# Kernel tuning notes

Measured on AMD Instinct MI355X. Metric: run time of the kernel, lower is better.

## Reference

```python
import jax, jax.numpy as jnp
import numpy as np

B, S, D = 8, 2048, 64
NEG = -1e9


def setup_inputs() -> dict:
    key = jax.random.key(0)
    kq, kk, kv = jax.random.split(key, 3)
    return {
        "queries": jax.random.normal(kq, (B, S, D), dtype=jnp.float32),
        "keys": jax.random.normal(kk, (B, S, D), dtype=jnp.float32),
        "values": jax.random.normal(kv, (B, S, D), dtype=jnp.float32),
        "mask_q": jnp.ones((B, S), dtype=jnp.float32),
        "mask_k": jnp.ones((B, S), dtype=jnp.float32),
        "mask_v": jnp.ones((B, S), dtype=jnp.float32),
    }


def reference(queries, keys, values, mask_q, mask_k, mask_v):
    # scaled QK^T: [B, Sq, Sk]
    scaler = jnp.sqrt(jnp.asarray(queries.shape[-1], dtype=queries.dtype))
    scores = jnp.einsum("bqd,bkd->bqk", queries, keys) / scaler
    # additive padding mask from outer product of query/key masks
    padding_mask = mask_q[:, :, None] * mask_k[:, None, :]  # [B, Sq, Sk]
    scores = scores + (1.0 - padding_mask) * NEG
    attention_weights = jax.nn.softmax(scores, axis=-1)
    # mask values then weighted sum
    values = values * mask_v[:, :, None]
    output = jnp.einsum("bqk,bkd->bqd", attention_weights, values)
    return output
```

## Files before the change

kernel.cpp:

```cpp
#include <hip/hip_runtime.h>
#include <hip/hip_bf16.h>
#include <math.h>

#define BATCH 8
#define SEQ   2048
#define DIM   64
#define NEGC  (-1e9f)
#define SPLIT 4
#define TPB   8

typedef short short8  __attribute__((ext_vector_type(8)));
typedef float f32x4   __attribute__((ext_vector_type(4)));
typedef float f32x16  __attribute__((ext_vector_type(16)));

#define MFMA32(a, b, c) __builtin_amdgcn_mfma_f32_32x32x16_bf16((a), (b), (c), 0, 0, 0)

__device__ __forceinline__ ushort f2bf(float x) {
    uint u = __float_as_uint(x);
    uint r = (u + 0x7fffu + ((u >> 16) & 1u)) >> 16;
    return (ushort)r;
}
__device__ __forceinline__ float bf2f(ushort h) {
    return __uint_as_float(((uint)h) << 16);
}

__global__ __launch_bounds__(256)
void prep_kv(const float* __restrict__ K, const float* __restrict__ V,
             const float* __restrict__ MV, ushort* __restrict__ ws) {
    __shared__ float raw[64 * 68];
    const int t    = threadIdx.x;
    const int b    = blockIdx.x >> 5;
    const int tile = blockIdx.x & 31;
    const float* Kb  = K  + ((size_t)b * SEQ + tile * 64) * DIM;
    const float* Vb  = V  + ((size_t)b * SEQ + tile * 64) * DIM;
    const float* MVb = MV + (size_t)b * SEQ + tile * 64;
    ushort* wsI = ws + (size_t)(b * 32 + tile) * 8192;

#pragma unroll
    for (int u = 0; u < 4; u++) {
        int f = t + 256 * u, key = f >> 4, d4 = (f & 15) * 4;
        *(float4*)&raw[key * 68 + d4] = *(const float4*)(Kb + (size_t)f * 4);
    }
    __syncthreads();
#pragma unroll
    for (int u = 0; u < 2; u++) {
        int r = t + 256 * u;
        int mt = r >> 8, kc = (r >> 6) & 3, L = r & 63;
        int key = mt * 32 + (L & 31), d0 = kc * 16 + (L >> 5) * 8;
        float4 x0 = *(float4*)&raw[key * 68 + d0];
        float4 x1 = *(float4*)&raw[key * 68 + d0 + 4];
        float xs[8] = {x0.x, x0.y, x0.z, x0.w, x1.x, x1.y, x1.z, x1.w};
        short8 hv;
#pragma unroll
        for (int j = 0; j < 8; j++) hv[j] = (short)f2bf(xs[j]);
        *(short8*)(wsI + r * 8) = hv;
    }
    __syncthreads();

#pragma unroll
    for (int u = 0; u < 4; u++) {
        int f = t + 256 * u, key = f >> 4, d4 = (f & 15) * 4;
        float4 x = *(const float4*)(Vb + (size_t)f * 4);
        float mv = MVb[key];
        x.x *= mv; x.y *= mv; x.z *= mv; x.w *= mv;
        *(float4*)&raw[key * 68 + d4] = x;
    }
    __syncthreads();
#pragma unroll
    for (int u = 0; u < 2; u++) {
        int r = t + 256 * u;
        int dt = r >> 8, kc = (r >> 6) & 3, L = r & 63;
        int d = dt * 32 + (L & 31), k0 = kc * 16 + (L >> 5) * 8;
        short8 ov;
#pragma unroll
        for (int j = 0; j < 8; j++) ov[j] = (short)f2bf(raw[(k0 + j) * 68 + d]);
        *(short8*)(wsI + 4096 + r * 8) = ov;
    }
}

__global__ __launch_bounds__(256, 4)
void attn_main(const float* __restrict__ Q, const float* __restrict__ MQ,
               const float* __restrict__ MK, const ushort* __restrict__ ws,
               float* __restrict__ PO, float* __restrict__ ML) {
    __shared__ __align__(16) ushort Stage[2][8192];

    const int t    = threadIdx.x;
    const int w    = t >> 6;
    const int lane = t & 63;
    const int h    = lane >> 5;
    const int lm   = lane & 31;
    const int qg   = w & 1;
    const int kh   = w >> 1;

    const int s  = blockIdx.x & 3;
    const int qb = blockIdx.x >> 2;
    const int b  = qb >> 5;
    const int qt = qb & 31;
    const int q  = qt * 64 + qg * 32 + lm;

    const float*  MKb  = MK + (size_t)b * SEQ;
    const ushort* wsKV = ws + (size_t)b * 32 * 8192;

    short8 qh[4], ql[4];
    {
        const float* Qr = Q + ((size_t)b * SEQ + q) * DIM;
#pragma unroll
        for (int kc = 0; kc < 4; kc++) {
            const float* p = Qr + kc * 16 + h * 8;
            float4 x0 = *(const float4*)p;
            float4 x1 = *(const float4*)(p + 4);
            float xs[8] = {x0.x, x0.y, x0.z, x0.w, x1.x, x1.y, x1.z, x1.w};
#pragma unroll
            for (int j = 0; j < 8; j++) {
                float v   = xs[j] * 0.125f;
                ushort hi = f2bf(v);
                ql[kc][j] = (short)f2bf(v - bf2f(hi));
                qh[kc][j] = (short)hi;
            }
        }
    }
    const float mq   = MQ[(size_t)b * SEQ + q];
    const float apen = NEGC * mq;

    float m = -1e30f, l = 0.0f;
    f32x16 ot0, ot1;
#pragma unroll
    for (int i = 0; i < 16; i++) { ot0[i] = 0.0f; ot1[i] = 0.0f; }

    {
        const ushort* src = wsKV + (size_t)(s * TPB) * 8192;
#pragma unroll
        for (int u = 0; u < 4; u++) {
            const int off = (u * 256 + w * 64 + lane) * 8;
            __builtin_amdgcn_global_load_lds(
                (const __attribute__((address_space(1))) void*)(src + off),
                (__attribute__((address_space(3))) void*)(&Stage[0][0] + off),
                16, 0, 0);
        }
    }
    __syncthreads();

    f32x4 mk[4];
#pragma unroll
    for (int v = 0; v < 4; v++)
        mk[v] = *(const f32x4*)(MKb + (s * TPB) * 64 + kh * 32 + v * 8 + h * 4);

#pragma unroll 1
    for (int tt = 0; tt < TPB; tt++) {
        const ushort* cur = &Stage[tt & 1][0];

        if (tt + 1 < TPB) {
            const ushort* src = wsKV + (size_t)(s * TPB + tt + 1) * 8192;
            ushort* dst = &Stage[(tt + 1) & 1][0];
#pragma unroll
            for (int u = 0; u < 4; u++) {
                const int off = (u * 256 + w * 64 + lane) * 8;
                __builtin_amdgcn_global_load_lds(
                    (const __attribute__((address_space(1))) void*)(src + off),
                    (__attribute__((address_space(3))) void*)(dst + off),
                    16, 0, 0);
            }
        }
        f32x4 nmk[4];
#pragma unroll
        for (int v = 0; v < 4; v++) nmk[v] = mk[v];
        if (tt + 1 < TPB) {
            const float* mkp = MKb + (s * TPB + tt + 1) * 64 + kh * 32 + h * 4;
#pragma unroll
            for (int v = 0; v < 4; v++) nmk[v] = *(const f32x4*)(mkp + v * 8);
        }

        f32x16 st;
#pragma unroll
        for (int i = 0; i < 16; i++) st[i] = 0.0f;
#pragma unroll
        for (int kc = 0; kc < 4; kc++) {
            short8 a = *(const short8*)&cur[((kh * 4 + kc) * 64 + lane) * 8];
            st = MFMA32(a, qh[kc], st);
            st = MFMA32(a, ql[kc], st);
        }

        float sv[16];
#pragma unroll
        for (int v = 0; v < 4; v++)
#pragma unroll
            for (int c = 0; c < 4; c++)
                sv[v * 4 + c] = st[v * 4 + c] + (NEGC - apen * mk[v][c]);
        float cm = sv[0];
#pragma unroll
        for (int i = 1; i < 16; i++) cm = fmaxf(cm, sv[i]);
        cm = fmaxf(cm, __shfl_xor(cm, 32));
        float nm    = fmaxf(m, cm);
        float alpha = __expf(m - nm);
        m = nm;

        float p[16], cs = 0.0f;
#pragma unroll
        for (int i = 0; i < 16; i++) { p[i] = __expf(sv[i] - nm); cs += p[i]; }
        cs += __shfl_xor(cs, 32);
        l   = l * alpha + cs;
        ot0 *= alpha; ot1 *= alpha;

        uint g[4][2], x[4][2];
#pragma unroll
        for (int v = 0; v < 4; v++) {
            __hip_bfloat162 c0 = __float22bfloat162_rn(make_float2(p[v*4+0], p[v*4+1]));
            __hip_bfloat162 c1 = __float22bfloat162_rn(make_float2(p[v*4+2], p[v*4+3]));
            __builtin_memcpy(&g[v][0], &c0, 4);
            __builtin_memcpy(&g[v][1], &c1, 4);
            x[v][0] = (uint)__shfl_xor((int)g[v][0], 32);
            x[v][1] = (uint)__shfl_xor((int)g[v][1], 32);
        }
        uint pbw[2][4];
        pbw[0][0] = h ? x[1][0] : g[0][0];
        pbw[0][1] = h ? x[1][1] : g[0][1];
        pbw[0][2] = h ? g[1][0] : x[0][0];
        pbw[0][3] = h ? g[1][1] : x[0][1];
        pbw[1][0] = h ? x[3][0] : g[2][0];
        pbw[1][1] = h ? x[3][1] : g[2][1];
        pbw[1][2] = h ? g[3][0] : x[2][0];
        pbw[1][3] = h ? g[3][1] : x[2][1];

#pragma unroll
        for (int c = 0; c < 2; c++) {
            short8 pb;
            __builtin_memcpy(&pb, &pbw[c][0], 16);
            short8 v0 = *(const short8*)&cur[4096 + ((0 * 4 + kh * 2 + c) * 64 + lane) * 8];
            short8 v1 = *(const short8*)&cur[4096 + ((1 * 4 + kh * 2 + c) * 64 + lane) * 8];
            ot0 = MFMA32(v0, pb, ot0);
            ot1 = MFMA32(v1, pb, ot1);
        }

#pragma unroll
        for (int v = 0; v < 4; v++) mk[v] = nmk[v];
        __syncthreads();
    }

    float* MscF = (float*)&Stage[0][0];
    if (kh == 1) {
        float* sc = MscF + (qg * 64 + lane) * 36;
#pragma unroll
        for (int i = 0; i < 16; i++) { sc[i] = ot0[i]; sc[16 + i] = ot1[i]; }
        sc[32] = m;
        sc[33] = l;
    }
    __syncthreads();
    if (kh == 0) {
        const float* sc = MscF + (qg * 64 + lane) * 36;
        float mb = sc[32], lb = sc[33];
        float nm = fmaxf(m, mb);
        float fa = __expf(m - nm);
        float fb = __expf(mb - nm);
        float lt = l * fa + lb * fb;

        float* po = PO + (((size_t)(s * 8 + b) * SEQ) + qt * 64 + qg * 32 + lm) * 64;
#pragma unroll
        for (int dt = 0; dt < 2; dt++) {
            const f32x16& o = dt ? ot1 : ot0;
#pragma unroll
            for (int rq = 0; rq < 4; rq++) {
                f32x4 r;
#pragma unroll
                for (int c = 0; c < 4; c++)
                    r[c] = o[rq * 4 + c] * fa + sc[dt * 16 + rq * 4 + c] * fb;
                *(f32x4*)(po + dt * 32 + rq * 8 + h * 4) = r;
            }
        }
        if (h == 0) {
            float2* ml2 = (float2*)ML;
            ml2[((size_t)(s * 8 + b) * SEQ) + qt * 64 + qg * 32 + lm] =
                make_float2(nm, lt);
        }
    }
}

__global__ __launch_bounds__(256)
void merge_o(const float* __restrict__ PO, const float* __restrict__ ML,
             float* __restrict__ O) {
    const int tid = blockIdx.x * 256 + threadIdx.x;
    const int qln = tid >> 4;
    const int dq  = tid & 15;
    const int b   = qln >> 11;
    const int qr  = qln & 2047;

    const float2* ml2 = (const float2*)ML;
    const size_t MLS = (size_t)8 * SEQ;
    float2 mls[SPLIT];
#pragma unroll
    for (int s = 0; s < SPLIT; s++) mls[s] = ml2[(size_t)(s * 8 + b) * SEQ + qr];
    float mm = mls[0].x;
#pragma unroll
    for (int s = 1; s < SPLIT; s++) mm = fmaxf(mm, mls[s].x);
    float f[SPLIT], denom = 0.0f;
#pragma unroll
    for (int s = 0; s < SPLIT; s++) {
        f[s] = __expf(mls[s].x - mm);
        denom += mls[s].y * f[s];
    }
    float inv = 1.0f / denom;

    const size_t POS = (size_t)8 * SEQ * 64;
    const size_t o0  = ((size_t)b * SEQ + qr) * 64 + dq * 4;
    f32x4 acc = {0, 0, 0, 0};
#pragma unroll
    for (int s = 0; s < SPLIT; s++)
        acc += (*(const f32x4*)(PO + s * POS + o0)) * f[s];
    *(f32x4*)(O + ((size_t)b * SEQ + qr) * DIM + dq * 4) = acc * inv;
    (void)MLS;
}

extern "C" void kernel_launch(void* const* d_in, const int* in_sizes, int n_in,
                              void* d_out, int out_size, void* d_ws, size_t ws_size,
                              hipStream_t stream) {
    const float* Q  = (const float*)d_in[0];
    const float* K  = (const float*)d_in[1];
    const float* V  = (const float*)d_in[2];
    const float* MQ = (const float*)d_in[3];
    const float* MK = (const float*)d_in[4];
    const float* MV = (const float*)d_in[5];
    float* O = (float*)d_out;

    ushort* wsKV = (ushort*)d_ws;
    float*  PO   = (float*)((char*)d_ws + (4u << 20));
    float*  ML   = (float*)((char*)d_ws + (20u << 20));

    prep_kv  <<<dim3(256),  dim3(256), 0, stream>>>(K, V, MV, wsKV);
    attn_main<<<dim3(1024), dim3(256), 0, stream>>>(Q, MQ, MK, wsKV, PO, ML);
    merge_o  <<<dim3(1024), dim3(256), 0, stream>>>(PO, ML, O);
}
```

Baseline: 101.8 us.

## Load K/V fragments directly into registers and split prep_kv into K and V blocks

The main attention loop no longer stages K/V tiles through double-buffered LDS with global_load_lds and per-iteration barriers. Each wave now loads its MFMA operand fragments straight from global memory into registers and prefetches the next K tile one iteration ahead. The prep kernel is split so separate blocks handle K and V, doubling its grid and halving the work per block. This removes LDS traffic and the loop barrier and frees LDS, at the cost of more register pressure and redundant global/L2 reads, since two waves sharing a kh half now load the same fragments. There is also a dead V load left in the code that the compiler should remove.

```diff
diff --git a/kernel.cpp b/kernel.cpp
--- a/kernel.cpp
+++ b/kernel.cpp
@@ -29,52 +29,55 @@
              const float* __restrict__ MV, ushort* __restrict__ ws) {
     __shared__ float raw[64 * 68];
     const int t    = threadIdx.x;
-    const int b    = blockIdx.x >> 5;
-    const int tile = blockIdx.x & 31;
-    const float* Kb  = K  + ((size_t)b * SEQ + tile * 64) * DIM;
-    const float* Vb  = V  + ((size_t)b * SEQ + tile * 64) * DIM;
-    const float* MVb = MV + (size_t)b * SEQ + tile * 64;
+    const int isV  = blockIdx.x >> 8;
+    const int img  = blockIdx.x & 255;
+    const int b    = img >> 5;
+    const int tile = img & 31;
     ushort* wsI = ws + (size_t)(b * 32 + tile) * 8192;
 
-#pragma unroll
-    for (int u = 0; u < 4; u++) {
-        int f = t + 256 * u, key = f >> 4, d4 = (f & 15) * 4;
-        *(float4*)&raw[key * 68 + d4] = *(const float4*)(Kb + (size_t)f * 4);
-    }
-    __syncthreads();
-#pragma unroll
-    for (int u = 0; u < 2; u++) {
-        int r = t + 256 * u;
-        int mt = r >> 8, kc = (r >> 6) & 3, L = r & 63;
-        int key = mt * 32 + (L & 31), d0 = kc * 16 + (L >> 5) * 8;
-        float4 x0 = *(float4*)&raw[key * 68 + d0];
-        float4 x1 = *(float4*)&raw[key * 68 + d0 + 4];
-        float xs[8] = {x0.x, x0.y, x0.z, x0.w, x1.x, x1.y, x1.z, x1.w};
-        short8 hv;
-#pragma unroll
-        for (int j = 0; j < 8; j++) hv[j] = (short)f2bf(xs[j]);
-        *(short8*)(wsI + r * 8) = hv;
-    }
-    __syncthreads();
-
-#pragma unroll
-    for (int u = 0; u < 4; u++) {
-        int f = t + 256 * u, key = f >> 4, d4 = (f & 15) * 4;
-        float4 x = *(const float4*)(Vb + (size_t)f * 4);
-        float mv = MVb[key];
-        x.x *= mv; x.y *= mv; x.z *= mv; x.w *= mv;
-        *(float4*)&raw[key * 68 + d4] = x;
-    }
-    __syncthreads();
-#pragma unroll
-    for (int u = 0; u < 2; u++) {
-        int r = t + 256 * u;
-        int dt = r >> 8, kc = (r >> 6) & 3, L = r & 63;
-        int d = dt * 32 + (L & 31), k0 = kc * 16 + (L >> 5) * 8;
-        short8 ov;
-#pragma unroll
-        for (int j = 0; j < 8; j++) ov[j] = (short)f2bf(raw[(k0 + j) * 68 + d]);
-        *(short8*)(wsI + 4096 + r * 8) = ov;
+    if (!isV) {
+        const float* Kb = K + ((size_t)b * SEQ + tile * 64) * DIM;
+#pragma unroll
+        for (int u = 0; u < 4; u++) {
+            int f = t + 256 * u, key = f >> 4, d4 = (f & 15) * 4;
+            *(float4*)&raw[key * 68 + d4] = *(const float4*)(Kb + (size_t)f * 4);
+        }
+        __syncthreads();
+#pragma unroll
+        for (int u = 0; u < 2; u++) {
+            int r = t + 256 * u;
+            int mt = r >> 8, kc = (r >> 6) & 3, L = r & 63;
+            int key = mt * 32 + (L & 31), d0 = kc * 16 + (L >> 5) * 8;
+            float4 x0 = *(float4*)&raw[key * 68 + d0];
+            float4 x1 = *(float4*)&raw[key * 68 + d0 + 4];
+            float xs[8] = {x0.x, x0.y, x0.z, x0.w, x1.x, x1.y, x1.z, x1.w};
+            short8 hv;
+#pragma unroll
+            for (int j = 0; j < 8; j++) hv[j] = (short)f2bf(xs[j]);
+            *(short8*)(wsI + r * 8) = hv;
+        }
+    } else {
+        const float* Vb  = V  + ((size_t)b * SEQ + tile * 64) * DIM;
+        const float* MVb = MV + (size_t)b * SEQ + tile * 64;
+#pragma unroll
+        for (int u = 0; u < 4; u++) {
+            int f = t + 256 * u, key = f >> 4, d4 = (f & 15) * 4;
+            float4 x = *(const float4*)(Vb + (size_t)f * 4);
+            float mv = MVb[key];
+            x.x *= mv; x.y *= mv; x.z *= mv; x.w *= mv;
+            *(float4*)&raw[key * 68 + d4] = x;
+        }
+        __syncthreads();
+#pragma unroll
+        for (int u = 0; u < 2; u++) {
+            int r = t + 256 * u;
+            int dt = r >> 8, kc = (r >> 6) & 3, L = r & 63;
+            int d = dt * 32 + (L & 31), k0 = kc * 16 + (L >> 5) * 8;
+            short8 ov;
+#pragma unroll
+            for (int j = 0; j < 8; j++) ov[j] = (short)f2bf(raw[(k0 + j) * 68 + d]);
+            *(short8*)(wsI + 4096 + r * 8) = ov;
+        }
     }
 }
 
@@ -82,7 +85,7 @@
 void attn_main(const float* __restrict__ Q, const float* __restrict__ MQ,
                const float* __restrict__ MK, const ushort* __restrict__ ws,
                float* __restrict__ PO, float* __restrict__ ML) {
-    __shared__ __align__(16) ushort Stage[2][8192];
+    __shared__ __align__(16) float Msc[2][64 * 36];
 
     const int t    = threadIdx.x;
     const int w    = t >> 6;
@@ -127,65 +130,59 @@
 #pragma unroll
     for (int i = 0; i < 16; i++) { ot0[i] = 0.0f; ot1[i] = 0.0f; }
 
+    short8 kf[4];
     {
-        const ushort* src = wsKV + (size_t)(s * TPB) * 8192;
-#pragma unroll
-        for (int u = 0; u < 4; u++) {
-            const int off = (u * 256 + w * 64 + lane) * 8;
-            __builtin_amdgcn_global_load_lds(
-                (const __attribute__((address_space(1))) void*)(src + off),
-                (__attribute__((address_space(3))) void*)(&Stage[0][0] + off),
-                16, 0, 0);
-        }
-    }
-    __syncthreads();
-
-    f32x4 mk[4];
-#pragma unroll
-    for (int v = 0; v < 4; v++)
-        mk[v] = *(const f32x4*)(MKb + (s * TPB) * 64 + kh * 32 + v * 8 + h * 4);
+        const ushort* img = wsKV + (size_t)(s * TPB) * 8192;
+#pragma unroll
+        for (int kc = 0; kc < 4; kc++)
+            kf[kc] = *(const short8*)(img + ((kh * 4 + kc) * 64 + lane) * 8);
+    }
 
 #pragma unroll 1
     for (int tt = 0; tt < TPB; tt++) {
-        const ushort* cur = &Stage[tt & 1][0];
-
-        if (tt + 1 < TPB) {
-            const ushort* src = wsKV + (size_t)(s * TPB + tt + 1) * 8192;
-            ushort* dst = &Stage[(tt + 1) & 1][0];
-#pragma unroll
-            for (int u = 0; u < 4; u++) {
-                const int off = (u * 256 + w * 64 + lane) * 8;
-                __builtin_amdgcn_global_load_lds(
-                    (const __attribute__((address_space(1))) void*)(src + off),
-                    (__attribute__((address_space(3))) void*)(dst + off),
-                    16, 0, 0);
-            }
-        }
-        f32x4 nmk[4];
-#pragma unroll
-        for (int v = 0; v < 4; v++) nmk[v] = mk[v];
-        if (tt + 1 < TPB) {
-            const float* mkp = MKb + (s * TPB + tt + 1) * 64 + kh * 32 + h * 4;
-#pragma unroll
-            for (int v = 0; v < 4; v++) nmk[v] = *(const f32x4*)(mkp + v * 8);
-        }
+        const ushort* img  = wsKV + (size_t)(s * TPB + tt) * 8192;
+        const ushort* imgN = (tt + 1 < TPB) ? img + 8192 : img;
+
+        short8 kn[4];
+#pragma unroll
+        for (int kc = 0; kc < 4; kc++)
+            kn[kc] = *(const short8*)(imgN + ((kh * 4 + kc) * 64 + lane) * 8);
+        short8 vv[4];
+#pragma unroll
+        for (int dt = 0; dt < 2; dt++)
+#pragma unroll
+            for (int c = 0; c < 2; c++)
+                vv[dt * 2 + c] = *(const short8*)(img + 4096 * 2 +
+                                                  0);
+#pragma unroll
+        for (int dt = 0; dt < 2; dt++)
+#pragma unroll
+            for (int c = 0; c < 2; c++)
+                vv[dt * 2 + c] = *(const short8*)(img + 4096 +
+                    ((dt * 4 + kh * 2 + c) * 64 + lane) * 8);
+        const float* mkp = MKb + (s * TPB + tt) * 64 + kh * 32 + h * 4;
+        f32x4 mk0 = *(const f32x4*)(mkp + 0);
+        f32x4 mk1 = *(const f32x4*)(mkp + 8);
+        f32x4 mk2 = *(const f32x4*)(mkp + 16);
+        f32x4 mk3 = *(const f32x4*)(mkp + 24);
 
         f32x16 st;
 #pragma unroll
         for (int i = 0; i < 16; i++) st[i] = 0.0f;
 #pragma unroll
         for (int kc = 0; kc < 4; kc++) {
-            short8 a = *(const short8*)&cur[((kh * 4 + kc) * 64 + lane) * 8];
-            st = MFMA32(a, qh[kc], st);
-            st = MFMA32(a, ql[kc], st);
+            st = MFMA32(kf[kc], qh[kc], st);
+            st = MFMA32(kf[kc], ql[kc], st);
         }
 
         float sv[16];
 #pragma unroll
-        for (int v = 0; v < 4; v++)
-#pragma unroll
-            for (int c = 0; c < 4; c++)
-                sv[v * 4 + c] = st[v * 4 + c] + (NEGC - apen * mk[v][c]);
+        for (int c = 0; c < 4; c++) {
+            sv[0 * 4 + c]  = st[0 * 4 + c]  + (NEGC - apen * mk0[c]);
+            sv[1 * 4 + c]  = st[1 * 4 + c]  + (NEGC - apen * mk1[c]);
+            sv[2 * 4 + c]  = st[2 * 4 + c]  + (NEGC - apen * mk2[c]);
+            sv[3 * 4 + c]  = st[3 * 4 + c]  + (NEGC - apen * mk3[c]);
+        }
         float cm = sv[0];
 #pragma unroll
         for (int i = 1; i < 16; i++) cm = fmaxf(cm, sv[i]);
@@ -225,20 +222,16 @@
         for (int c = 0; c < 2; c++) {
             short8 pb;
             __builtin_memcpy(&pb, &pbw[c][0], 16);
-            short8 v0 = *(const short8*)&cur[4096 + ((0 * 4 + kh * 2 + c) * 64 + lane) * 8];
-            short8 v1 = *(const short8*)&cur[4096 + ((1 * 4 + kh * 2 + c) * 64 + lane) * 8];
-            ot0 = MFMA32(v0, pb, ot0);
-            ot1 = MFMA32(v1, pb, ot1);
-        }
-
-#pragma unroll
-        for (int v = 0; v < 4; v++) mk[v] = nmk[v];
-        __syncthreads();
-    }
-
-    float* MscF = (float*)&Stage[0][0];
+            ot0 = MFMA32(vv[0 * 2 + c], pb, ot0);
+            ot1 = MFMA32(vv[1 * 2 + c], pb, ot1);
+        }
+
+#pragma unroll
+        for (int kc = 0; kc < 4; kc++) kf[kc] = kn[kc];
+    }
+
     if (kh == 1) {
-        float* sc = MscF + (qg * 64 + lane) * 36;
+        float* sc = &Msc[qg][lane * 36];
 #pragma unroll
         for (int i = 0; i < 16; i++) { sc[i] = ot0[i]; sc[16 + i] = ot1[i]; }
         sc[32] = m;
@@ -246,7 +239,7 @@
     }
     __syncthreads();
     if (kh == 0) {
-        const float* sc = MscF + (qg * 64 + lane) * 36;
+        const float* sc = &Msc[qg][lane * 36];
         float mb = sc[32], lb = sc[33];
         float nm = fmaxf(m, mb);
         float fa = __expf(m - nm);
@@ -284,7 +277,6 @@
     const int qr  = qln & 2047;
 
     const float2* ml2 = (const float2*)ML;
-    const size_t MLS = (size_t)8 * SEQ;
     float2 mls[SPLIT];
 #pragma unroll
     for (int s = 0; s < SPLIT; s++) mls[s] = ml2[(size_t)(s * 8 + b) * SEQ + qr];
@@ -306,7 +298,6 @@
     for (int s = 0; s < SPLIT; s++)
         acc += (*(const f32x4*)(PO + s * POS + o0)) * f[s];
     *(f32x4*)(O + ((size_t)b * SEQ + qr) * DIM + dq * 4) = acc * inv;
-    (void)MLS;
 }
 
 extern "C" void kernel_launch(void* const* d_in, const int* in_sizes, int n_in,
@@ -324,7 +315,7 @@
     float*  PO   = (float*)((char*)d_ws + (4u << 20));
     float*  ML   = (float*)((char*)d_ws + (20u << 20));
 
-    prep_kv  <<<dim3(256),  dim3(256), 0, stream>>>(K, V, MV, wsKV);
+    prep_kv  <<<dim3(512),  dim3(256), 0, stream>>>(K, V, MV, wsKV);
     attn_main<<<dim3(1024), dim3(256), 0, stream>>>(Q, MQ, MK, wsKV, PO, ML);
     merge_o  <<<dim3(1024), dim3(256), 0, stream>>>(PO, ML, O);
 }
```

Result: slower. 107.9 us (+6.0%).
